# Kernel tuning notes

Hardware: AMD Instinct MI355X
Metric: run time of the kernel (lower is better)

Reference implementation:

```python
import jax, jax.numpy as jnp
import numpy as np

N, D, E, H, O, K = 4096, 1024, 8, 4096, 1024, 2
LOSS_COEF = 0.01


def setup_inputs() -> dict:
    key = jax.random.key(0)
    ks = jax.random.split(key, 4)
    scale = lambda k, shape, fan: (jax.random.normal(k, shape, jnp.float32) / np.sqrt(fan).astype(np.float32))
    return {
        "x": jax.random.normal(ks[0], (N, D), jnp.float32),
        "Wg": scale(ks[1], (D, E), D),            # gating network
        "W1": scale(ks[2], (E, D, H), D),          # stacked expert layer 1
        "b1": jnp.zeros((E, H), jnp.float32),
        "W2": scale(ks[3], (E, H, O), H),          # stacked expert layer 2
        "b2": jnp.zeros((E, O), jnp.float32),
        "k": K,
    }


def _cv_squared(v):
    # coefficient-of-variation squared, the tensor2tensor load-balancing loss
    eps = jnp.asarray(1e-10, v.dtype)
    m = jnp.mean(v)
    return jnp.var(v) / (m * m + eps)


def reference(x, Wg, W1, b1, W2, b2, k):
    n, e = x.shape[0], Wg.shape[1]
    # --- top-k gating (deterministic / inference path) ---
    logits = x @ Wg                               # [N, E]
    top_vals, top_idx = jax.lax.top_k(logits, k)  # [N, k]
    top_gates = jax.nn.softmax(top_vals, axis=-1)
    gates = jnp.zeros((n, e), x.dtype).at[jnp.arange(n)[:, None], top_idx].set(top_gates)  # [N, E], sparse rows
    # --- expert compute (dense grouped form of dispatch->expert->combine) ---
    h = jax.nn.relu(jnp.einsum('nd,edh->enh', x, W1) + b1[:, None, :])  # [E, N, H]
    y = jnp.einsum('enh,eho->eno', h, W2) + b2[:, None, :]               # [E, N, O]
    out = jnp.einsum('ne,eno->no', gates, y)                              # weighted combine [N, O]
    # --- auxiliary load-balancing loss ---
    importance = gates.sum(axis=0)                # [E]
    aux_loss = LOSS_COEF * _cv_squared(importance)
    return out, aux_loss
```

## Files before the change

kernel.cpp:

```cpp
#include <hip/hip_runtime.h>
#include <hip/hip_bf16.h>
#include <stdint.h>

#define N_TOK 4096
#define DIM   1024
#define NE    8
#define HID   4096
#define OUTD  1024
#define TOPK  2
#define SLOTS (N_TOK*TOPK)

typedef __bf16 bf16_t;
typedef __attribute__((ext_vector_type(8))) __bf16 bf16x8;
typedef __attribute__((ext_vector_type(4))) __bf16 bf16x4;
typedef __attribute__((ext_vector_type(4))) float  f32x4;

static __device__ __forceinline__ uint32_t pk2(float a, float b) {
    __bf16 x = (__bf16)a, y = (__bf16)b;
    return (uint32_t)__builtin_bit_cast(uint16_t, x) |
          ((uint32_t)__builtin_bit_cast(uint16_t, y) << 16);
}

__global__ __launch_bounds__(512)
void k_gating(const float* __restrict__ x, const float* __restrict__ wg,
              bf16_t* __restrict__ xb,
              int* __restrict__ tki, float* __restrict__ tkg) {
    int n = blockIdx.x * 8 + (threadIdx.x >> 6);
    int lane = threadIdx.x & 63;
    const float* xr = x + (size_t)n * DIM;
    double acc[NE];
#pragma unroll
    for (int e = 0; e < NE; ++e) acc[e] = 0.0;
#pragma unroll
    for (int i = 0; i < 4; ++i) {
        int d0 = i * 256 + lane * 4;
        float4 v = *(const float4*)&xr[d0];
        bf16x4 o;
        o[0] = (__bf16)v.x; o[1] = (__bf16)v.y; o[2] = (__bf16)v.z; o[3] = (__bf16)v.w;
        *(bf16x4*)&xb[(size_t)n * DIM + d0] = o;
        const float* wr = wg + (size_t)d0 * NE;
#pragma unroll
        for (int j = 0; j < 4; ++j) {
            double xv = (double)((&v.x)[j]);
#pragma unroll
            for (int e = 0; e < NE; ++e) acc[e] += xv * (double)wr[j * NE + e];
        }
    }
#pragma unroll
    for (int e = 0; e < NE; ++e)
        for (int off = 32; off > 0; off >>= 1) acc[e] += __shfl_xor(acc[e], off);
    if (lane == 0) {
        int i0 = 0; double v0 = acc[0];
#pragma unroll
        for (int e = 1; e < NE; ++e) if (acc[e] > v0) { v0 = acc[e]; i0 = e; }
        int i1 = -1; double v1 = -1e300;
#pragma unroll
        for (int e = 0; e < NE; ++e) if (e != i0 && acc[e] > v1) { v1 = acc[e]; i1 = e; }
        double e1 = exp(v1 - v0);
        double s = 1.0 + e1;
        tki[n*2]   = i0;  tki[n*2+1] = i1;
        tkg[n*2]   = (float)(1.0 / s);
        tkg[n*2+1] = (float)(e1 / s);
    }
}

__global__ void k_count(const int* __restrict__ tki, const float* __restrict__ tkg,
                        int* __restrict__ counts, float* __restrict__ imp) {
    int e = blockIdx.x, t = threadIdx.x;
    __shared__ int   rc[256];
    __shared__ float rg[256];
    int c = 0; float g = 0.f;
    for (int i = t; i < SLOTS; i += 256)
        if (tki[i] == e) { ++c; g += tkg[i]; }
    rc[t] = c; rg[t] = g; __syncthreads();
    for (int off = 128; off > 0; off >>= 1) {
        if (t < off) { rc[t] += rc[t + off]; rg[t] += rg[t + off]; }
        __syncthreads();
    }
    if (t == 0) { counts[e] = rc[0]; imp[e] = rg[0]; }
}

__global__ void k_finalize(const float* __restrict__ imp, const int* __restrict__ counts,
                           int* __restrict__ bases, float* __restrict__ aux_out) {
    if (threadIdx.x == 0 && blockIdx.x == 0) {
        float m = 0.f;
        for (int e = 0; e < NE; ++e) m += imp[e];
        m /= (float)NE;
        float var = 0.f;
        for (int e = 0; e < NE; ++e) { float d = imp[e] - m; var += d * d; }
        var /= (float)NE;
        aux_out[0] = 0.01f * var / (m * m + 1e-10f);
        int b = 0;
        for (int e = 0; e < NE; ++e) { bases[e] = b; b += counts[e]; }
    }
}

__global__ __launch_bounds__(256)
void k_place(const int* __restrict__ tki, const int* __restrict__ bases,
             int* __restrict__ tok_ids, int* __restrict__ slotmap) {
    int e = blockIdx.x, t = threadIdx.x;
    int wid = t >> 6, lane = t & 63;
    __shared__ int wc[4];
    int run = bases[e];
    for (int base = 0; base < SLOTS; base += 256) {
        int i = base + t;
        bool f = (tki[i] == e);
        unsigned long long b = __ballot(f);
        int pre = __popcll(b & ((1ull << lane) - 1ull));
        if (lane == 0) wc[wid] = __popcll(b);
        __syncthreads();
        int woff = 0;
#pragma unroll
        for (int u = 0; u < 4; ++u) if (u < wid) woff += wc[u];
        int tot = wc[0] + wc[1] + wc[2] + wc[3];
        if (f) { int s = run + woff + pre; tok_ids[s] = i >> 1; slotmap[i] = s; }
        run += tot;
        __syncthreads();
    }
}

__global__ __launch_bounds__(512)
void k_transpose(const float* __restrict__ w1, const float* __restrict__ w2,
                 bf16_t* __restrict__ w1t, bf16_t* __restrict__ w2t) {
    __shared__ bf16_t tT[64][264];
    const int bx = blockIdx.x;
    const float* src; bf16_t* dst; int R, C, ry, cx;
    if (bx < 2048) {
        int e = bx >> 8, rem = bx & 255;
        ry = rem >> 6; cx = rem & 63;
        src = w1 + (size_t)e * DIM * HID; dst = w1t + (size_t)e * DIM * HID;
        R = DIM; C = HID;
    } else {
        int b2 = bx - 2048;
        int e = b2 >> 8, rem = b2 & 255;
        ry = rem >> 4; cx = rem & 15;
        src = w2 + (size_t)e * HID * OUTD; dst = w2t + (size_t)e * HID * OUTD;
        R = HID; C = OUTD;
    }
    const int r0 = ry * 256, c0 = cx * 64;
    const int tx = threadIdx.x & 15;
    const int ta = threadIdx.x >> 4;
#pragma unroll
    for (int p = 0; p < 4; ++p) {
        int r = 2 * ta + 64 * p;
        float4 va = *(const float4*)&src[(size_t)(r0 + r)     * C + c0 + tx * 4];
        float4 vb = *(const float4*)&src[(size_t)(r0 + r + 1) * C + c0 + tx * 4];
#pragma unroll
        for (int j = 0; j < 4; ++j)
            *(uint32_t*)&tT[tx * 4 + j][r] = pk2((&va.x)[j], (&vb.x)[j]);
    }
    __syncthreads();
    const int w = threadIdx.x >> 6, l = threadIdx.x & 63;
    const int ccb = w * 2 + (l >> 5);
    const int rb  = (l & 31) * 8;
#pragma unroll
    for (int q = 0; q < 4; ++q) {
        int cc = q * 16 + ccb;
        bf16x8 o = *(const bf16x8*)&tT[cc][rb];
        *(bf16x8*)&dst[(size_t)(c0 + cc) * R + r0 + rb] = o;
    }
}

template <int MODE>
__global__ __launch_bounds__(512, 2)
void k_gemm(const bf16_t* __restrict__ A,
            const bf16_t* __restrict__ Bt,
            const float* __restrict__ bias,
            const int* __restrict__ tok_ids,
            const int* __restrict__ bases,
            const int* __restrict__ counts,
            bf16_t* __restrict__ Y) {
    constexpr int KD   = (MODE == 0) ? DIM : HID;
    constexpr int ND   = (MODE == 0) ? HID : OUTD;
    constexpr int KLEN = (MODE == 0) ? DIM : (HID / 2);
    constexpr int KT   = KLEN / 32;
    constexpr int BUFE = 16384;

    const int e  = blockIdx.x & 7;
    const int lb = blockIdx.x >> 3;
    const int ne = counts[e];
    if (ne == 0) return;
    const int b0 = bases[e];
    const int NTy = (ne + 255) >> 8;
    const int NTILES = (MODE == 0) ? (16 * NTy) : (8 * NTy);

    extern __shared__ bf16_t lds[];

    const int t = threadIdx.x, w = t >> 6, L = t & 63;
    const int wm = w >> 2, wn = w & 3;
    const int lr = L & 15, lq = L >> 4;
    const int srow  = L >> 2;
    const int sslot = L & 3;

    int offA[8], offB[4];
#pragma unroll
    for (int i = 0; i < 8; ++i) {
        int r = wm * 128 + i * 16 + lr;
        offA[i] = r * 32 + ((lq ^ ((r >> 1) & 3)) << 3);
    }
#pragma unroll
    for (int j = 0; j < 4; ++j) {
        int r = wn * 64 + j * 16 + lr;
        offB[j] = 8192 + r * 32 + ((lq ^ ((r >> 1) & 3)) << 3);
    }
    int sdstA[2], sdstB[2];
#pragma unroll
    for (int g = 0; g < 2; ++g) {
        sdstA[g] = (g * 128 + w * 16) * 32;
        sdstB[g] = 8192 + (g * 128 + w * 16) * 32;
    }

#define GLL(srcp, dste) __builtin_amdgcn_global_load_lds( \
        (const __attribute__((address_space(1))) uint32_t*)(srcp), \
        (__attribute__((address_space(3))) uint32_t*)(lds + (dste)), 16, 0, 0)
#define STAGE(Tt, bsl) { \
        _Pragma("unroll") for (int g_ = 0; g_ < 2; ++g_) { \
            GLL(aptr[g_] + (Tt) * 32, (bsl) * BUFE + sdstA[g_]); \
            GLL(bptr[g_] + (Tt) * 32, (bsl) * BUFE + sdstB[g_]); } }

    for (int ti = lb; ti < NTILES; ti += 32) {
        int panel = ti / NTy, y = ti - panel * NTy, kslot = 0;
        if (MODE == 1) { kslot = panel & 1; panel >>= 1; }
        const int m0 = y * 256, n0 = panel * 256;
        const int koff = (MODE == 0) ? 0 : kslot * KLEN;
        bf16_t* __restrict__ Yw = (MODE == 0) ? Y : (Y + (size_t)kslot * SLOTS * OUTD);

        const bf16_t* aptr[2];
        const bf16_t* bptr[2];
#pragma unroll
        for (int g = 0; g < 2; ++g) {
            int row = g * 128 + w * 16 + srow;
            int gk  = sslot ^ ((row >> 1) & 3);
            int mm = m0 + row;
            int rr = (mm < ne) ? mm : (ne - 1);
            size_t arow = (MODE == 0) ? (size_t)tok_ids[b0 + rr] * KD : (size_t)(b0 + rr) * KD;
            aptr[g] = A + arow + koff + gk * 8;
            bptr[g] = Bt + ((size_t)e * ND + n0 + row) * KD + koff + gk * 8;
        }

        f32x4 acc[8][4];
#pragma unroll
        for (int i = 0; i < 8; ++i)
#pragma unroll
            for (int j = 0; j < 4; ++j) acc[i][j] = (f32x4){0.f, 0.f, 0.f, 0.f};

        __builtin_amdgcn_s_barrier();

        STAGE(0, 0); STAGE(1, 1);

        int cb = 0;
        int nb = 2;
        for (int T = 0; T < KT; ++T) {
            if (T < KT - 1) { asm volatile("s_waitcnt vmcnt(4)" ::: "memory"); }
            else            { asm volatile("s_waitcnt vmcnt(0)" ::: "memory"); }
            __builtin_amdgcn_s_barrier();
            if (T + 2 < KT) STAGE(T + 2, nb);

            bf16x8 fb[4], fa[8];
#pragma unroll
            for (int j = 0; j < 4; ++j) fb[j] = *(const bf16x8*)(lds + cb * BUFE + offB[j]);
#pragma unroll
            for (int i = 0; i < 4; ++i) fa[i] = *(const bf16x8*)(lds + cb * BUFE + offA[i]);
            __builtin_amdgcn_sched_barrier(0);
#pragma unroll
            for (int i = 4; i < 8; ++i) fa[i] = *(const bf16x8*)(lds + cb * BUFE + offA[i]);
            __builtin_amdgcn_sched_barrier(0);
            asm volatile("s_waitcnt lgkmcnt(4)" ::: "memory");
            __builtin_amdgcn_sched_barrier(0);
            __builtin_amdgcn_s_setprio(1);
#pragma unroll
            for (int i = 0; i < 4; ++i)
#pragma unroll
                for (int j = 0; j < 4; ++j)
                    acc[i][j] = __builtin_amdgcn_mfma_f32_16x16x32_bf16(fb[j], fa[i], acc[i][j], 0, 0, 0);
            __builtin_amdgcn_s_setprio(0);
            asm volatile("s_waitcnt lgkmcnt(0)" ::: "memory");
            __builtin_amdgcn_sched_barrier(0);
            __builtin_amdgcn_s_setprio(1);
#pragma unroll
            for (int i = 4; i < 8; ++i)
#pragma unroll
                for (int j = 0; j < 4; ++j)
                    acc[i][j] = __builtin_amdgcn_mfma_f32_16x16x32_bf16(fb[j], fa[i], acc[i][j], 0, 0, 0);
            __builtin_amdgcn_s_setprio(0);

            cb = (cb == 2) ? 0 : cb + 1;
            nb = (nb == 2) ? 0 : nb + 1;
        }

        const int kbias = (MODE == 0) ? 1 : (kslot == 0 ? 1 : 0);
#pragma unroll
        for (int i = 0; i < 8; ++i) {
            int gm = m0 + wm * 128 + i * 16 + lr;
            if (gm < ne) {
#pragma unroll
                for (int j = 0; j < 4; ++j) {
                    int gn = n0 + wn * 64 + j * 16 + lq * 4;
                    f32x4 bv = *(const f32x4*)&bias[(size_t)e * ND + gn];
                    bf16x4 hv;
#pragma unroll
                    for (int r = 0; r < 4; ++r) {
                        float v = acc[i][j][r];
                        if (kbias) v += bv[r];
                        if (MODE == 0) v = fmaxf(v, 0.f);
                        hv[r] = (__bf16)v;
                    }
                    *(bf16x4*)&Yw[(size_t)(b0 + gm) * ND + gn] = hv;
                }
            }
        }
    }
#undef STAGE
#undef GLL
}

__global__ void k_combine(const bf16_t* __restrict__ ybuf,
                          const int* __restrict__ slotmap,
                          const float* __restrict__ tkg,
                          float* __restrict__ out) {
    int n = blockIdx.x;
    int d = threadIdx.x * 4;
    int s0 = slotmap[2 * n], s1 = slotmap[2 * n + 1];
    float g0 = tkg[2 * n],  g1 = tkg[2 * n + 1];
    const bf16_t* y2 = ybuf + (size_t)SLOTS * OUTD;
    bf16x4 a0 = *(const bf16x4*)&ybuf[(size_t)s0 * OUTD + d];
    bf16x4 a1 = *(const bf16x4*)&y2  [(size_t)s0 * OUTD + d];
    bf16x4 c0 = *(const bf16x4*)&ybuf[(size_t)s1 * OUTD + d];
    bf16x4 c1 = *(const bf16x4*)&y2  [(size_t)s1 * OUTD + d];
    f32x4 o;
#pragma unroll
    for (int r = 0; r < 4; ++r)
        o[r] = g0 * ((float)a0[r] + (float)a1[r]) + g1 * ((float)c0[r] + (float)c1[r]);
    *(f32x4*)&out[(size_t)n * OUTD + d] = o;
}

extern "C" void kernel_launch(void* const* d_in, const int* in_sizes, int n_in,
                              void* d_out, int out_size, void* d_ws, size_t ws_size,
                              hipStream_t stream) {
    const float* x  = (const float*)d_in[0];
    const float* wg = (const float*)d_in[1];
    const float* w1 = (const float*)d_in[2];
    const float* b1 = (const float*)d_in[3];
    const float* w2 = (const float*)d_in[4];
    const float* b2 = (const float*)d_in[5];
    float* out = (float*)d_out;

    char* ws = (char*)d_ws;
    size_t o = 0;
    auto alloc = [&](size_t b) { size_t r = o; o = (o + b + 255) & ~(size_t)255; return r; };
    int*    counts  = (int*)(ws + alloc(NE * 4));
    int*    bases   = (int*)(ws + alloc(NE * 4));
    float*  imp     = (float*)(ws + alloc(NE * 4));
    int*    tki     = (int*)(ws + alloc(SLOTS * 4));
    float*  tkg     = (float*)(ws + alloc(SLOTS * 4));
    int*    tok_ids = (int*)(ws + alloc(SLOTS * 4));
    int*    slotmap = (int*)(ws + alloc(SLOTS * 4));
    bf16_t* xb      = (bf16_t*)(ws + alloc((size_t)N_TOK * DIM * 2));
    size_t  w1t_off = alloc((size_t)NE * HID * DIM * 2);
    bf16_t* w1t     = (bf16_t*)(ws + w1t_off);
    bf16_t* ybuf    = (bf16_t*)(ws + w1t_off);
    bf16_t* w2t     = (bf16_t*)(ws + alloc((size_t)NE * OUTD * HID * 2));
    bf16_t* hbuf    = (bf16_t*)(ws + alloc((size_t)SLOTS * HID * 2));
    (void)ws_size; (void)n_in; (void)in_sizes;

    hipFuncSetAttribute((const void*)&k_gemm<0>, hipFuncAttributeMaxDynamicSharedMemorySize, 98304);
    hipFuncSetAttribute((const void*)&k_gemm<1>, hipFuncAttributeMaxDynamicSharedMemorySize, 98304);

    k_gating<<<N_TOK / 8, 512, 0, stream>>>(x, wg, xb, tki, tkg);
    k_count<<<NE, 256, 0, stream>>>(tki, tkg, counts, imp);
    k_finalize<<<1, 64, 0, stream>>>(imp, counts, bases, out + (size_t)N_TOK * OUTD);
    k_place<<<NE, 256, 0, stream>>>(tki, bases, tok_ids, slotmap);
    k_transpose<<<4096, 512, 0, stream>>>(w1, w2, w1t, w2t);

    k_gemm<0><<<256, 512, 98304, stream>>>(xb, w1t, b1, tok_ids, bases, counts, hbuf);
    k_gemm<1><<<256, 512, 98304, stream>>>(hbuf, w2t, b2, tok_ids, bases, counts, ybuf);

    k_combine<<<N_TOK, 256, 0, stream>>>(ybuf, slotmap, tkg, out);
}
```

Before: 358.3 us.

## Fuse routing kernels and flatten grouped GEMM into one tile per block

Merges the count, finalize and place kernels into a single routing kernel that also computes per-expert tile prefix offsets. The grouped GEMMs drop the persistent 32-blocks-per-expert loop and launch one block per tile over a flat tile list spanning all experts. This removes per-expert load imbalance and cuts two launches, at the cost of a tile-to-expert lookup per block and a fixed upper bound on grid size (640 and 320 tiles).

New measurement: 340.7 us. -4.9%, faster.

```diff
diff --git a/kernel.cpp b/kernel.cpp
--- a/kernel.cpp
+++ b/kernel.cpp
@@ -9,6 +9,8 @@
 #define OUTD  1024
 #define TOPK  2
 #define SLOTS (N_TOK*TOPK)
+#define MAXT0 640
+#define MAXT1 320
 
 typedef __bf16 bf16_t;
 typedef __attribute__((ext_vector_type(8))) __bf16 bf16x8;
@@ -64,50 +66,68 @@
     }
 }
 
-__global__ void k_count(const int* __restrict__ tki, const float* __restrict__ tkg,
-                        int* __restrict__ counts, float* __restrict__ imp) {
-    int e = blockIdx.x, t = threadIdx.x;
-    __shared__ int   rc[256];
-    __shared__ float rg[256];
-    int c = 0; float g = 0.f;
-    for (int i = t; i < SLOTS; i += 256)
-        if (tki[i] == e) { ++c; g += tkg[i]; }
-    rc[t] = c; rg[t] = g; __syncthreads();
-    for (int off = 128; off > 0; off >>= 1) {
-        if (t < off) { rc[t] += rc[t + off]; rg[t] += rg[t + off]; }
-        __syncthreads();
-    }
-    if (t == 0) { counts[e] = rc[0]; imp[e] = rg[0]; }
-}
-
-__global__ void k_finalize(const float* __restrict__ imp, const int* __restrict__ counts,
-                           int* __restrict__ bases, float* __restrict__ aux_out) {
-    if (threadIdx.x == 0 && blockIdx.x == 0) {
+__global__ __launch_bounds__(256)
+void k_route(const int* __restrict__ tki, const float* __restrict__ tkg,
+             int* __restrict__ counts, int* __restrict__ bases,
+             int* __restrict__ tb0, int* __restrict__ tb1,
+             float* __restrict__ aux_out,
+             int* __restrict__ tok_ids, int* __restrict__ slotmap) {
+    const int e = blockIdx.x, t = threadIdx.x;
+    const int wid = t >> 6, lane = t & 63;
+    int   lc[NE]; float lg[NE];
+#pragma unroll
+    for (int k = 0; k < NE; ++k) { lc[k] = 0; lg[k] = 0.f; }
+    for (int i = t; i < SLOTS; i += 256) {
+        int ee = tki[i]; float gg = tkg[i];
+#pragma unroll
+        for (int k = 0; k < NE; ++k) if (ee == k) { lc[k]++; lg[k] += gg; }
+    }
+#pragma unroll
+    for (int k = 0; k < NE; ++k)
+        for (int off = 32; off > 0; off >>= 1) {
+            lc[k] += __shfl_xor(lc[k], off);
+            lg[k] += __shfl_xor(lg[k], off);
+        }
+    __shared__ int   wcI[4][NE];
+    __shared__ float wcF[4][NE];
+    if (lane == 0)
+#pragma unroll
+        for (int k = 0; k < NE; ++k) { wcI[wid][k] = lc[k]; wcF[wid][k] = lg[k]; }
+    __syncthreads();
+    int cnt[NE];
+#pragma unroll
+    for (int k = 0; k < NE; ++k)
+        cnt[k] = wcI[0][k] + wcI[1][k] + wcI[2][k] + wcI[3][k];
+    if (e == 0 && t == 0) {
+        float gs[NE];
+#pragma unroll
+        for (int k = 0; k < NE; ++k)
+            gs[k] = wcF[0][k] + wcF[1][k] + wcF[2][k] + wcF[3][k];
         float m = 0.f;
-        for (int e = 0; e < NE; ++e) m += imp[e];
+        for (int k = 0; k < NE; ++k) m += gs[k];
         m /= (float)NE;
         float var = 0.f;
-        for (int e = 0; e < NE; ++e) { float d = imp[e] - m; var += d * d; }
+        for (int k = 0; k < NE; ++k) { float d = gs[k] - m; var += d * d; }
         var /= (float)NE;
         aux_out[0] = 0.01f * var / (m * m + 1e-10f);
-        int b = 0;
-        for (int e = 0; e < NE; ++e) { bases[e] = b; b += counts[e]; }
-    }
-}
-
-__global__ __launch_bounds__(256)
-void k_place(const int* __restrict__ tki, const int* __restrict__ bases,
-             int* __restrict__ tok_ids, int* __restrict__ slotmap) {
-    int e = blockIdx.x, t = threadIdx.x;
-    int wid = t >> 6, lane = t & 63;
+        int b = 0, c0 = 0, c1 = 0;
+        tb0[0] = 0; tb1[0] = 0;
+        for (int k = 0; k < NE; ++k) {
+            counts[k] = cnt[k]; bases[k] = b; b += cnt[k];
+            int nty = (cnt[k] + 255) >> 8;
+            c0 += 16 * nty; c1 += 8 * nty;
+            tb0[k+1] = c0; tb1[k+1] = c1;
+        }
+    }
+    int run = 0;
+    for (int k = 0; k < e; ++k) run += cnt[k];
     __shared__ int wc[4];
-    int run = bases[e];
     for (int base = 0; base < SLOTS; base += 256) {
         int i = base + t;
         bool f = (tki[i] == e);
-        unsigned long long b = __ballot(f);
-        int pre = __popcll(b & ((1ull << lane) - 1ull));
-        if (lane == 0) wc[wid] = __popcll(b);
+        unsigned long long bl = __ballot(f);
+        int pre = __popcll(bl & ((1ull << lane) - 1ull));
+        if (lane == 0) wc[wid] = __popcll(bl);
         __syncthreads();
         int woff = 0;
 #pragma unroll
@@ -169,6 +189,7 @@
             const int* __restrict__ tok_ids,
             const int* __restrict__ bases,
             const int* __restrict__ counts,
+            const int* __restrict__ tb,
             bf16_t* __restrict__ Y) {
     constexpr int KD   = (MODE == 0) ? DIM : HID;
     constexpr int ND   = (MODE == 0) ? HID : OUTD;
@@ -176,13 +197,20 @@
     constexpr int KT   = KLEN / 32;
     constexpr int BUFE = 16384;
 
-    const int e  = blockIdx.x & 7;
-    const int lb = blockIdx.x >> 3;
+    const int ti = blockIdx.x;
+    if (ti >= tb[NE]) return;
+    int e = 0;
+#pragma unroll
+    for (int k = 1; k < NE; ++k) if (ti >= tb[k]) e = k;
+    const int local = ti - tb[e];
     const int ne = counts[e];
-    if (ne == 0) return;
     const int b0 = bases[e];
-    const int NTy = (ne + 255) >> 8;
-    const int NTILES = (MODE == 0) ? (16 * NTy) : (8 * NTy);
+    int panel, y, kslot = 0;
+    if (MODE == 0) { y = local >> 4; panel = local & 15; }
+    else           { y = local >> 3; int q = local & 7; panel = q >> 1; kslot = q & 1; }
+    const int m0 = y * 256, n0 = panel * 256;
+    const int koff = (MODE == 0) ? 0 : kslot * KLEN;
+    bf16_t* __restrict__ Yw = (MODE == 0) ? Y : (Y + (size_t)kslot * SLOTS * OUTD);
 
     extern __shared__ bf16_t lds[];
 
@@ -218,95 +246,85 @@
             GLL(aptr[g_] + (Tt) * 32, (bsl) * BUFE + sdstA[g_]); \
             GLL(bptr[g_] + (Tt) * 32, (bsl) * BUFE + sdstB[g_]); } }
 
-    for (int ti = lb; ti < NTILES; ti += 32) {
-        int panel = ti / NTy, y = ti - panel * NTy, kslot = 0;
-        if (MODE == 1) { kslot = panel & 1; panel >>= 1; }
-        const int m0 = y * 256, n0 = panel * 256;
-        const int koff = (MODE == 0) ? 0 : kslot * KLEN;
-        bf16_t* __restrict__ Yw = (MODE == 0) ? Y : (Y + (size_t)kslot * SLOTS * OUTD);
-
-        const bf16_t* aptr[2];
-        const bf16_t* bptr[2];
-#pragma unroll
-        for (int g = 0; g < 2; ++g) {
-            int row = g * 128 + w * 16 + srow;
-            int gk  = sslot ^ ((row >> 1) & 3);
-            int mm = m0 + row;
-            int rr = (mm < ne) ? mm : (ne - 1);
-            size_t arow = (MODE == 0) ? (size_t)tok_ids[b0 + rr] * KD : (size_t)(b0 + rr) * KD;
-            aptr[g] = A + arow + koff + gk * 8;
-            bptr[g] = Bt + ((size_t)e * ND + n0 + row) * KD + koff + gk * 8;
-        }
-
-        f32x4 acc[8][4];
-#pragma unroll
-        for (int i = 0; i < 8; ++i)
-#pragma unroll
-            for (int j = 0; j < 4; ++j) acc[i][j] = (f32x4){0.f, 0.f, 0.f, 0.f};
-
+    const bf16_t* aptr[2];
+    const bf16_t* bptr[2];
+#pragma unroll
+    for (int g = 0; g < 2; ++g) {
+        int row = g * 128 + w * 16 + srow;
+        int gk  = sslot ^ ((row >> 1) & 3);
+        int mm = m0 + row;
+        int rr = (mm < ne) ? mm : (ne - 1);
+        size_t arow = (MODE == 0) ? (size_t)tok_ids[b0 + rr] * KD : (size_t)(b0 + rr) * KD;
+        aptr[g] = A + arow + koff + gk * 8;
+        bptr[g] = Bt + ((size_t)e * ND + n0 + row) * KD + koff + gk * 8;
+    }
+
+    f32x4 acc[8][4];
+#pragma unroll
+    for (int i = 0; i < 8; ++i)
+#pragma unroll
+        for (int j = 0; j < 4; ++j) acc[i][j] = (f32x4){0.f, 0.f, 0.f, 0.f};
+
+    STAGE(0, 0); STAGE(1, 1);
+
+    int cb = 0;
+    int nb = 2;
+    for (int T = 0; T < KT; ++T) {
+        if (T < KT - 1) { asm volatile("s_waitcnt vmcnt(4)" ::: "memory"); }
+        else            { asm volatile("s_waitcnt vmcnt(0)" ::: "memory"); }
         __builtin_amdgcn_s_barrier();
-
-        STAGE(0, 0); STAGE(1, 1);
-
-        int cb = 0;
-        int nb = 2;
-        for (int T = 0; T < KT; ++T) {
-            if (T < KT - 1) { asm volatile("s_waitcnt vmcnt(4)" ::: "memory"); }
-            else            { asm volatile("s_waitcnt vmcnt(0)" ::: "memory"); }
-            __builtin_amdgcn_s_barrier();
-            if (T + 2 < KT) STAGE(T + 2, nb);
-
-            bf16x8 fb[4], fa[8];
-#pragma unroll
-            for (int j = 0; j < 4; ++j) fb[j] = *(const bf16x8*)(lds + cb * BUFE + offB[j]);
-#pragma unroll
-            for (int i = 0; i < 4; ++i) fa[i] = *(const bf16x8*)(lds + cb * BUFE + offA[i]);
-            __builtin_amdgcn_sched_barrier(0);
-#pragma unroll
-            for (int i = 4; i < 8; ++i) fa[i] = *(const bf16x8*)(lds + cb * BUFE + offA[i]);
-            __builtin_amdgcn_sched_barrier(0);
-            asm volatile("s_waitcnt lgkmcnt(4)" ::: "memory");
-            __builtin_amdgcn_sched_barrier(0);
-            __builtin_amdgcn_s_setprio(1);
-#pragma unroll
-            for (int i = 0; i < 4; ++i)
-#pragma unroll
-                for (int j = 0; j < 4; ++j)
-                    acc[i][j] = __builtin_amdgcn_mfma_f32_16x16x32_bf16(fb[j], fa[i], acc[i][j], 0, 0, 0);
-            __builtin_amdgcn_s_setprio(0);
-            asm volatile("s_waitcnt lgkmcnt(0)" ::: "memory");
-            __builtin_amdgcn_sched_barrier(0);
-            __builtin_amdgcn_s_setprio(1);
-#pragma unroll
-            for (int i = 4; i < 8; ++i)
-#pragma unroll
-                for (int j = 0; j < 4; ++j)
-                    acc[i][j] = __builtin_amdgcn_mfma_f32_16x16x32_bf16(fb[j], fa[i], acc[i][j], 0, 0, 0);
-            __builtin_amdgcn_s_setprio(0);
-
-            cb = (cb == 2) ? 0 : cb + 1;
-            nb = (nb == 2) ? 0 : nb + 1;
-        }
-
-        const int kbias = (MODE == 0) ? 1 : (kslot == 0 ? 1 : 0);
-#pragma unroll
-        for (int i = 0; i < 8; ++i) {
-            int gm = m0 + wm * 128 + i * 16 + lr;
-            if (gm < ne) {
-#pragma unroll
-                for (int j = 0; j < 4; ++j) {
-                    int gn = n0 + wn * 64 + j * 16 + lq * 4;
-                    f32x4 bv = *(const f32x4*)&bias[(size_t)e * ND + gn];
-                    bf16x4 hv;
-#pragma unroll
-                    for (int r = 0; r < 4; ++r) {
-                        float v = acc[i][j][r];
-                        if (kbias) v += bv[r];
-                        if (MODE == 0) v = fmaxf(v, 0.f);
-                        hv[r] = (__bf16)v;
-                    }
-                    *(bf16x4*)&Yw[(size_t)(b0 + gm) * ND + gn] = hv;
+        if (T + 2 < KT) STAGE(T + 2, nb);
+
+        bf16x8 fb[4], fa[8];
+#pragma unroll
+        for (int j = 0; j < 4; ++j) fb[j] = *(const bf16x8*)(lds + cb * BUFE + offB[j]);
+#pragma unroll
+        for (int i = 0; i < 4; ++i) fa[i] = *(const bf16x8*)(lds + cb * BUFE + offA[i]);
+        __builtin_amdgcn_sched_barrier(0);
+#pragma unroll
+        for (int i = 4; i < 8; ++i) fa[i] = *(const bf16x8*)(lds + cb * BUFE + offA[i]);
+        __builtin_amdgcn_sched_barrier(0);
+        asm volatile("s_waitcnt lgkmcnt(4)" ::: "memory");
+        __builtin_amdgcn_sched_barrier(0);
+        __builtin_amdgcn_s_setprio(1);
+#pragma unroll
+        for (int i = 0; i < 4; ++i)
+#pragma unroll
+            for (int j = 0; j < 4; ++j)
+                acc[i][j] = __builtin_amdgcn_mfma_f32_16x16x32_bf16(fb[j], fa[i], acc[i][j], 0, 0, 0);
+        __builtin_amdgcn_s_setprio(0);
+        asm volatile("s_waitcnt lgkmcnt(0)" ::: "memory");
+        __builtin_amdgcn_sched_barrier(0);
+        __builtin_amdgcn_s_setprio(1);
+#pragma unroll
+        for (int i = 4; i < 8; ++i)
+#pragma unroll
+            for (int j = 0; j < 4; ++j)
+                acc[i][j] = __builtin_amdgcn_mfma_f32_16x16x32_bf16(fb[j], fa[i], acc[i][j], 0, 0, 0);
+        __builtin_amdgcn_s_setprio(0);
+
+        cb = (cb == 2) ? 0 : cb + 1;
+        nb = (nb == 2) ? 0 : nb + 1;
+    }
+
+    const int kbias = (MODE == 0) ? 1 : (kslot == 0 ? 1 : 0);
+#pragma unroll
+    for (int i = 0; i < 8; ++i) {
+        int gm = m0 + wm * 128 + i * 16 + lr;
+        if (gm < ne) {
+#pragma unroll
+            for (int j = 0; j < 4; ++j) {
+                int gn = n0 + wn * 64 + j * 16 + lq * 4;
+                f32x4 bv = *(const f32x4*)&bias[(size_t)e * ND + gn];
+                bf16x4 hv;
+#pragma unroll
+                for (int r = 0; r < 4; ++r) {
+                    float v = acc[i][j][r];
+                    if (kbias) v += bv[r];
+                    if (MODE == 0) v = fmaxf(v, 0.f);
+                    hv[r] = (__bf16)v;
                 }
+                *(bf16x4*)&Yw[(size_t)(b0 + gm) * ND + gn] = hv;
             }
         }
     }
@@ -350,7 +368,8 @@
     auto alloc = [&](size_t b) { size_t r = o; o = (o + b + 255) & ~(size_t)255; return r; };
     int*    counts  = (int*)(ws + alloc(NE * 4));
     int*    bases   = (int*)(ws + alloc(NE * 4));
-    float*  imp     = (float*)(ws + alloc(NE * 4));
+    int*    tb0     = (int*)(ws + alloc((NE + 1) * 4));
+    int*    tb1     = (int*)(ws + alloc((NE + 1) * 4));
     int*    tki     = (int*)(ws + alloc(SLOTS * 4));
     float*  tkg     = (float*)(ws + alloc(SLOTS * 4));
     int*    tok_ids = (int*)(ws + alloc(SLOTS * 4));
@@ -367,13 +386,12 @@
     hipFuncSetAttribute((const void*)&k_gemm<1>, hipFuncAttributeMaxDynamicSharedMemorySize, 98304);
 
     k_gating<<<N_TOK / 8, 512, 0, stream>>>(x, wg, xb, tki, tkg);
-    k_count<<<NE, 256, 0, stream>>>(tki, tkg, counts, imp);
-    k_finalize<<<1, 64, 0, stream>>>(imp, counts, bases, out + (size_t)N_TOK * OUTD);
-    k_place<<<NE, 256, 0, stream>>>(tki, bases, tok_ids, slotmap);
+    k_route<<<NE, 256, 0, stream>>>(tki, tkg, counts, bases, tb0, tb1,
+                                    out + (size_t)N_TOK * OUTD, tok_ids, slotmap);
     k_transpose<<<4096, 512, 0, stream>>>(w1, w2, w1t, w2t);
 
-    k_gemm<0><<<256, 512, 98304, stream>>>(xb, w1t, b1, tok_ids, bases, counts, hbuf);
-    k_gemm<1><<<256, 512, 98304, stream>>>(hbuf, w2t, b2, tok_ids, bases, counts, ybuf);
+    k_gemm<0><<<MAXT0, 512, 98304, stream>>>(xb, w1t, b1, tok_ids, bases, counts, tb0, hbuf);
+    k_gemm<1><<<MAXT1, 512, 98304, stream>>>(hbuf, w2t, b2, tok_ids, bases, counts, tb1, ybuf);
 
     k_combine<<<N_TOK, 256, 0, stream>>>(ybuf, slotmap, tkg, out);
 }
```
